# Performance work log

Measured on AMD Instinct MI355X. Metric: run time of the kernel, lower is better.

The kernel has to match this reference:

```python
import jax, jax.numpy as jnp
import numpy as np

B, S, D, H, M, K = 2048, 32, 1024, 1024, 4096, 32


def setup_inputs() -> dict:
    key = jax.random.key(0)
    ks = jax.random.split(key, 10)
    inp = {
        "x": jax.random.normal(ks[0], (B, S, D), dtype=jnp.float32),
        "topk": K,
        "W_enc": jax.random.normal(ks[1], (D, H), dtype=jnp.float32) * (1.0 / np.sqrt(D)),
        "b_enc": jnp.zeros((H,), dtype=jnp.float32),
        "w_curv": jax.random.normal(ks[2], (H, 1), dtype=jnp.float32) * (1.0 / np.sqrt(H)),
        "b_curv": jnp.zeros((1,), dtype=jnp.float32),
        "memory_slots": jax.random.normal(ks[3], (M, H), dtype=jnp.float32),
        "assoc": jax.random.normal(ks[4], (M, M), dtype=jnp.float32) * 0.01,
        "W_dec": jax.random.normal(ks[5], (H, D), dtype=jnp.float32) * (1.0 / np.sqrt(H)),
        "b_dec": jnp.zeros((D,), dtype=jnp.float32),
        "temperature": jnp.asarray(1.0, dtype=jnp.float32),
    }
    return inp


def reference(x, topk, W_enc, b_enc, w_curv, b_curv, memory_slots, assoc, W_dec, b_dec, temperature):
    # encoder + pooled query
    enc = jnp.tanh(x @ W_enc + b_enc)          # [B,S,H]
    query = enc.mean(axis=1)                   # [B,H]

    # content-based addressing (active_slots == M, temperature buffer)
    sim = jnp.einsum('bd,md->bm', query, memory_slots)        # [B,M]
    gate = jax.nn.sigmoid(query @ w_curv + b_curv)            # [B,1]
    sim = sim * (0.5 + gate) / jnp.maximum(temperature, 1e-6)
    vals, idx = jax.lax.top_k(sim, topk)                      # [B,K], sorted desc (matches torch.topk)

    # associative activation: two rounds of softmax -> assoc matmul
    act = jnp.einsum('bd,md->bm', query, memory_slots)        # [B,M]
    for _ in range(2):
        act = jax.nn.softmax(act, axis=-1) @ assoc

    # combine top-k scores with gathered associative activations
    comb = jax.nn.softmax(vals + jnp.take_along_axis(act, idx, axis=1), axis=-1)  # [B,K]
    mem = memory_slots[idx]                                   # [B,K,H] gather
    read = jnp.einsum('bk,bkh->bh', comb, mem)                # [B,H]

    out = jnp.tanh(read @ W_dec + b_dec)                      # [B,D]
    return jnp.broadcast_to(out[:, None, :], (x.shape[0], x.shape[1], out.shape[-1]))
```

## Files before the change

kernel.cpp:

```cpp
#include <hip/hip_runtime.h>

typedef _Float16 f16;
typedef f16 f16x8 __attribute__((ext_vector_type(8)));
typedef float f32x4 __attribute__((ext_vector_type(4)));

#define BD 2048
#define SD 32
#define DD 1024
#define HD 1024
#define MD 4096
#define KD 32
#define PADK 40

__global__ void k_transpose_f16(const float* __restrict__ in, f16* __restrict__ out,
                                int R, int C) {
  __shared__ float tile[32][33];
  int c0 = blockIdx.x * 32, r0 = blockIdx.y * 32;
  int tx = threadIdx.x & 31, ty = threadIdx.x >> 5;
#pragma unroll
  for (int i = 0; i < 4; ++i) {
    int r = ty + i * 8;
    tile[r][tx] = in[(size_t)(r0 + r) * C + c0 + tx];
  }
  __syncthreads();
#pragma unroll
  for (int i = 0; i < 4; ++i) {
    int r = ty + i * 8;
    out[(size_t)(c0 + r) * R + r0 + tx] = (f16)tile[tx][r];
  }
}

__global__ void k_transpose_split(const float* __restrict__ in, f16* __restrict__ outHi,
                                  f16* __restrict__ outLo, int R, int C) {
  __shared__ float tile[32][33];
  int c0 = blockIdx.x * 32, r0 = blockIdx.y * 32;
  int tx = threadIdx.x & 31, ty = threadIdx.x >> 5;
#pragma unroll
  for (int i = 0; i < 4; ++i) {
    int r = ty + i * 8;
    tile[r][tx] = in[(size_t)(r0 + r) * C + c0 + tx];
  }
  __syncthreads();
#pragma unroll
  for (int i = 0; i < 4; ++i) {
    int r = ty + i * 8;
    float v = tile[tx][r];
    f16 h = (f16)v;
    size_t o = (size_t)(c0 + r) * R + r0 + tx;
    outHi[o] = h;
    outLo[o] = (f16)(v - (float)h);
  }
}

__global__ void k_split(const float* __restrict__ in, f16* __restrict__ hi,
                        f16* __restrict__ lo, int n8) {
  int i = blockIdx.x * 256 + threadIdx.x;
  if (i >= n8) return;
  const float4* p = (const float4*)in + (size_t)i * 2;
  float4 a = p[0], b = p[1];
  float v[8] = {a.x, a.y, a.z, a.w, b.x, b.y, b.z, b.w};
  f16x8 h, l;
#pragma unroll
  for (int e = 0; e < 8; ++e) {
    h[e] = (f16)v[e];
    l[e] = (f16)(v[e] - (float)h[e]);
  }
  *((f16x8*)hi + i) = h;
  *((f16x8*)lo + i) = l;
}

template <int SPLIT, int EPI>
__global__ __launch_bounds__(256) void k_gemm_nt(const void* __restrict__ Ap,
                                                 const f16* __restrict__ Bhi,
                                                 const f16* __restrict__ Blo,
                                                 float* __restrict__ C,
                                                 const float* __restrict__ bias,
                                                 int M, int N, int K) {
  __shared__ f16 As[128 * PADK];
  __shared__ f16 Bs[128 * PADK];
  __shared__ f16 Asl[SPLIT ? 128 * PADK : 8];
  __shared__ f16 Bsl[SPLIT ? 128 * PADK : 8];
  const int n0 = blockIdx.x * 128, m0 = blockIdx.y * 128;
  const int t = threadIdx.x;
  const int lane = t & 63, w = t >> 6;
  const int wm = w >> 1, wn = w & 1;
  const int quad = lane >> 4, l16 = lane & 15;
  const int srow = t >> 2, sseg = t & 3;

  f32x4 acc[4][4] = {};

  for (int kc = 0; kc < K; kc += 32) {
#pragma unroll
    for (int rep = 0; rep < 2; ++rep) {
      int row = srow + rep * 64;
      if (SPLIT) {
        const float* g = (const float*)Ap + (size_t)(m0 + row) * K + kc + sseg * 8;
        float4 u0 = *(const float4*)g;
        float4 u1 = *(const float4*)(g + 4);
        float v[8] = {u0.x, u0.y, u0.z, u0.w, u1.x, u1.y, u1.z, u1.w};
        f16x8 h, l;
#pragma unroll
        for (int e = 0; e < 8; ++e) {
          h[e] = (f16)v[e];
          l[e] = (f16)(v[e] - (float)h[e]);
        }
        *(f16x8*)(As + row * PADK + sseg * 8) = h;
        *(f16x8*)(Asl + row * PADK + sseg * 8) = l;
        size_t bo = (size_t)(n0 + row) * K + kc + sseg * 8;
        *(f16x8*)(Bs + row * PADK + sseg * 8) = *(const f16x8*)(Bhi + bo);
        *(f16x8*)(Bsl + row * PADK + sseg * 8) = *(const f16x8*)(Blo + bo);
      } else {
        const f16* g = (const f16*)Ap + (size_t)(m0 + row) * K + kc + sseg * 8;
        *(f16x8*)(As + row * PADK + sseg * 8) = *(const f16x8*)g;
        const f16* gb = Bhi + (size_t)(n0 + row) * K + kc + sseg * 8;
        *(f16x8*)(Bs + row * PADK + sseg * 8) = *(const f16x8*)gb;
      }
    }
    __syncthreads();
    f16x8 ah[4], bh[4];
#pragma unroll
    for (int i = 0; i < 4; ++i) {
      ah[i] = *(const f16x8*)(As + (wm * 64 + i * 16 + l16) * PADK + quad * 8);
      bh[i] = *(const f16x8*)(Bs + (wn * 64 + i * 16 + l16) * PADK + quad * 8);
    }
    if (SPLIT) {
      f16x8 al[4], bl[4];
#pragma unroll
      for (int i = 0; i < 4; ++i) {
        al[i] = *(const f16x8*)(Asl + (wm * 64 + i * 16 + l16) * PADK + quad * 8);
        bl[i] = *(const f16x8*)(Bsl + (wn * 64 + i * 16 + l16) * PADK + quad * 8);
      }
#pragma unroll
      for (int i = 0; i < 4; ++i)
#pragma unroll
        for (int j = 0; j < 4; ++j) {
          acc[i][j] = __builtin_amdgcn_mfma_f32_16x16x32_f16(ah[i], bh[j], acc[i][j], 0, 0, 0);
          acc[i][j] = __builtin_amdgcn_mfma_f32_16x16x32_f16(ah[i], bl[j], acc[i][j], 0, 0, 0);
          acc[i][j] = __builtin_amdgcn_mfma_f32_16x16x32_f16(al[i], bh[j], acc[i][j], 0, 0, 0);
        }
    } else {
#pragma unroll
      for (int i = 0; i < 4; ++i)
#pragma unroll
        for (int j = 0; j < 4; ++j)
          acc[i][j] = __builtin_amdgcn_mfma_f32_16x16x32_f16(ah[i], bh[j], acc[i][j], 0, 0, 0);
    }
    __syncthreads();
  }

  if (EPI == 0) {
#pragma unroll
    for (int i = 0; i < 4; ++i) {
#pragma unroll
      for (int j = 0; j < 4; ++j) {
        int row = m0 + wm * 64 + i * 16 + quad * 4;
        int col = n0 + wn * 64 + j * 16 + l16;
        float* cp = C + (size_t)row * N + col;
#pragma unroll
        for (int r = 0; r < 4; ++r) cp[(size_t)r * N] = acc[i][j][r];
      }
    }
  } else if (EPI == 2) {
#pragma unroll
    for (int i = 0; i < 4; ++i) {
#pragma unroll
      for (int j = 0; j < 4; ++j) {
        int row = m0 + wm * 64 + i * 16 + quad * 4;
        int col = n0 + wn * 64 + j * 16 + l16;
        float bv = bias[col];
        float* cp = C + (size_t)row * N + col;
#pragma unroll
        for (int r = 0; r < 4; ++r) cp[(size_t)r * N] = tanhf(acc[i][j][r] + bv);
      }
    }
  } else {
#pragma unroll
    for (int j = 0; j < 4; ++j) {
      int col = n0 + wn * 64 + j * 16 + l16;
      float bv = bias[col];
      float g0 = 0.f, g1 = 0.f;
#pragma unroll
      for (int i = 0; i < 4; ++i) {
        float s = 0.f;
#pragma unroll
        for (int r = 0; r < 4; ++r) s += tanhf(acc[i][j][r] + bv);
        if (i < 2) g0 += s; else g1 += s;
      }
      g0 += __shfl_xor(g0, 16); g0 += __shfl_xor(g0, 32);
      g1 += __shfl_xor(g1, 16); g1 += __shfl_xor(g1, 32);
      if (quad == 0) {
        int grp = (m0 + wm * 64) >> 5;
        C[(size_t)grp * N + col] = g0 * (1.0f / 32.0f);
        C[(size_t)(grp + 1) * N + col] = g1 * (1.0f / 32.0f);
      }
    }
  }
}

__global__ void k_gate(const float* __restrict__ query, const float* __restrict__ w_curv,
                       const float* __restrict__ b_curv, const float* __restrict__ temp,
                       float* __restrict__ scale) {
  int b = blockIdx.x, t = threadIdx.x;
  float s = 0.f;
  for (int h = t; h < HD; h += 256) s += query[(size_t)b * HD + h] * w_curv[h];
#pragma unroll
  for (int off = 32; off; off >>= 1) s += __shfl_xor(s, off);
  __shared__ float red[4];
  if ((t & 63) == 0) red[t >> 6] = s;
  __syncthreads();
  if (t == 0) {
    float tot = red[0] + red[1] + red[2] + red[3] + b_curv[0];
    float g = 1.f / (1.f + expf(-tot));
    scale[b] = (0.5f + g) / fmaxf(temp[0], 1e-6f);
  }
}

__global__ void k_topk(const float* __restrict__ sim, const float* __restrict__ scale,
                       int* __restrict__ idx, float* __restrict__ vals) {
  int b = blockIdx.x, t = threadIdx.x;
  __shared__ float sv[MD];
  __shared__ float rv[4];
  __shared__ int ri[4];
  for (int i = t; i < MD; i += 256) sv[i] = sim[(size_t)b * MD + i];
  __syncthreads();
  float sc = scale[b];
  for (int k = 0; k < KD; ++k) {
    float bv = -1e30f;
    int bi = 0x7fffffff;
    for (int i = t; i < MD; i += 256) {
      float v = sv[i];
      if (v > bv) { bv = v; bi = i; }
    }
#pragma unroll
    for (int off = 1; off < 64; off <<= 1) {
      float ov = __shfl_xor(bv, off);
      int oi = __shfl_xor(bi, off);
      if (ov > bv || (ov == bv && oi < bi)) { bv = ov; bi = oi; }
    }
    if ((t & 63) == 0) { rv[t >> 6] = bv; ri[t >> 6] = bi; }
    __syncthreads();
    if (t == 0) {
      float fv = rv[0];
      int fi = ri[0];
#pragma unroll
      for (int u = 1; u < 4; ++u)
        if (rv[u] > fv || (rv[u] == fv && ri[u] < fi)) { fv = rv[u]; fi = ri[u]; }
      idx[b * KD + k] = fi;
      vals[b * KD + k] = fv * sc;
      sv[fi] = -1e30f;
    }
    __syncthreads();
  }
}

__global__ void k_softmax(const float* __restrict__ in, f16* __restrict__ out, int C) {
  int b = blockIdx.x, t = threadIdx.x;
  const float* row = in + (size_t)b * C;
  __shared__ float red[4];
  float m = -1e30f;
  for (int i = t; i < C; i += 256) m = fmaxf(m, row[i]);
#pragma unroll
  for (int off = 32; off; off >>= 1) m = fmaxf(m, __shfl_xor(m, off));
  if ((t & 63) == 0) red[t >> 6] = m;
  __syncthreads();
  m = fmaxf(fmaxf(red[0], red[1]), fmaxf(red[2], red[3]));
  __syncthreads();
  float s = 0.f;
  for (int i = t; i < C; i += 256) s += expf(row[i] - m);
#pragma unroll
  for (int off = 32; off; off >>= 1) s += __shfl_xor(s, off);
  if ((t & 63) == 0) red[t >> 6] = s;
  __syncthreads();
  s = red[0] + red[1] + red[2] + red[3];
  float inv = 1.f / s;
  for (int i = t; i < C; i += 256) out[(size_t)b * C + i] = (f16)(expf(row[i] - m) * inv);
}

__global__ void k_combine(const float* __restrict__ vals, const int* __restrict__ idx,
                          const float* __restrict__ act, const float* __restrict__ mem,
                          f16* __restrict__ read_h) {
  int b = blockIdx.x, t = threadIdx.x;
  __shared__ float comb[KD];
  __shared__ int sidx[KD];
  if (t < KD) {
    int id = idx[b * KD + t];
    sidx[t] = id;
    float e = vals[b * KD + t] + act[(size_t)b * MD + id];
    float m = e;
#pragma unroll
    for (int off = 16; off; off >>= 1) m = fmaxf(m, __shfl_xor(m, off));
    float p = expf(e - m);
    float s = p;
#pragma unroll
    for (int off = 16; off; off >>= 1) s += __shfl_xor(s, off);
    comb[t] = p / s;
  }
  __syncthreads();
  for (int h = t; h < HD; h += 256) {
    float a = 0.f;
#pragma unroll
    for (int k = 0; k < KD; ++k) a += comb[k] * mem[(size_t)sidx[k] * HD + h];
    read_h[(size_t)b * HD + h] = (f16)a;
  }
}

__global__ void k_broadcast(const float4* __restrict__ src, float4* __restrict__ dst) {
  size_t v = (size_t)blockIdx.x * 256 + threadIdx.x;
  size_t d4 = v & 255;
  size_t b = v >> 13;
  dst[v] = src[b * 256 + d4];
}

extern "C" void kernel_launch(void* const* d_in, const int* in_sizes, int n_in,
                              void* d_out, int out_size, void* d_ws, size_t ws_size,
                              hipStream_t stream) {
  const float* x      = (const float*)d_in[0];
  const float* W_enc  = (const float*)d_in[2];
  const float* b_enc  = (const float*)d_in[3];
  const float* w_curv = (const float*)d_in[4];
  const float* b_curv = (const float*)d_in[5];
  const float* mem    = (const float*)d_in[6];
  const float* assoc  = (const float*)d_in[7];
  const float* W_dec  = (const float*)d_in[8];
  const float* b_dec  = (const float*)d_in[9];
  const float* temp   = (const float*)d_in[10];
  float* out = (float*)d_out;

  char* ws = (char*)d_ws;
  size_t off = 0;
  auto alloc = [&](size_t bytes) {
    void* p = ws + off;
    off += (bytes + 255) & ~(size_t)255;
    return p;
  };
  f16* Wt_hi   = (f16*)alloc((size_t)HD * DD * 2);
  f16* Wt_lo   = (f16*)alloc((size_t)HD * DD * 2);
  f16* ms_hi   = (f16*)alloc((size_t)MD * HD * 2);
  f16* ms_lo   = (f16*)alloc((size_t)MD * HD * 2);
  f16* assocT  = (f16*)alloc((size_t)MD * MD * 2);
  f16* WdT     = (f16*)alloc((size_t)DD * HD * 2);
  float* query = (float*)alloc((size_t)BD * HD * 4);
  float* scale = (float*)alloc((size_t)BD * 4);
  float* sim   = (float*)alloc((size_t)BD * MD * 4);
  int* idx     = (int*)alloc((size_t)BD * KD * 4);
  float* vals  = (float*)alloc((size_t)BD * KD * 4);
  f16* p_h     = (f16*)alloc((size_t)BD * MD * 2);
  f16* read_h  = (f16*)alloc((size_t)BD * HD * 2);
  float* out_b = (float*)alloc((size_t)BD * DD * 4);
  (void)ws_size; (void)in_sizes; (void)n_in; (void)out_size;

  dim3 b256(256);
  k_transpose_split<<<dim3(HD / 32, DD / 32), b256, 0, stream>>>(W_enc, Wt_hi, Wt_lo, DD, HD);
  k_split<<<dim3((MD * HD / 8 + 255) / 256), b256, 0, stream>>>(mem, ms_hi, ms_lo, MD * HD / 8);
  k_transpose_f16<<<dim3(MD / 32, MD / 32), b256, 0, stream>>>(assoc, assocT, MD, MD);
  k_transpose_f16<<<dim3(DD / 32, HD / 32), b256, 0, stream>>>(W_dec, WdT, HD, DD);
  k_gemm_nt<1, 1><<<dim3(HD / 128, BD * SD / 128), b256, 0, stream>>>(
      x, Wt_hi, Wt_lo, query, b_enc, BD * SD, HD, DD);
  k_gate<<<dim3(BD), b256, 0, stream>>>(query, w_curv, b_curv, temp, scale);
  k_gemm_nt<1, 0><<<dim3(MD / 128, BD / 128), b256, 0, stream>>>(
      query, ms_hi, ms_lo, sim, nullptr, BD, MD, HD);
  k_topk<<<dim3(BD), b256, 0, stream>>>(sim, scale, idx, vals);
  k_softmax<<<dim3(BD), b256, 0, stream>>>(sim, p_h, MD);
  k_gemm_nt<0, 0><<<dim3(MD / 128, BD / 128), b256, 0, stream>>>(
      p_h, assocT, nullptr, sim, nullptr, BD, MD, MD);
  k_softmax<<<dim3(BD), b256, 0, stream>>>(sim, p_h, MD);
  k_gemm_nt<0, 0><<<dim3(MD / 128, BD / 128), b256, 0, stream>>>(
      p_h, assocT, nullptr, sim, nullptr, BD, MD, MD);
  k_combine<<<dim3(BD), b256, 0, stream>>>(vals, idx, sim, mem, read_h);
  k_gemm_nt<0, 2><<<dim3(DD / 128, BD / 128), b256, 0, stream>>>(
      read_h, WdT, nullptr, out_b, b_dec, BD, DD, HD);
  k_broadcast<<<dim3(BD * SD * DD / 1024), b256, 0, stream>>>(
      (const float4*)out_b, (float4*)out);
}
```

Before: 1.461 ms.

## Prepack B operands in MFMA fragment layout and fuse decoder broadcast

Weights and memory slots are prepacked into the per-lane MFMA fragment order, so the GEMM loads B fragments straight from global memory into registers and no longer stages them through LDS. The A tile in LDS uses an XOR swizzle instead of padding to avoid bank conflicts. The final decoder GEMM writes the tanh output broadcast across S directly, which removes the intermediate buffer and the separate broadcast kernel. The trade-off is that B fragments are now read from global memory by every wave without LDS sharing, which adds cache traffic. The fused epilogue also writes its output with strided, less coalesced stores.

```diff
diff --git a/kernel.cpp b/kernel.cpp
--- a/kernel.cpp
+++ b/kernel.cpp
@@ -10,89 +10,87 @@
 #define HD 1024
 #define MD 4096
 #define KD 32
-#define PADK 40
-
-__global__ void k_transpose_f16(const float* __restrict__ in, f16* __restrict__ out,
-                                int R, int C) {
-  __shared__ float tile[32][33];
-  int c0 = blockIdx.x * 32, r0 = blockIdx.y * 32;
-  int tx = threadIdx.x & 31, ty = threadIdx.x >> 5;
-#pragma unroll
-  for (int i = 0; i < 4; ++i) {
-    int r = ty + i * 8;
-    tile[r][tx] = in[(size_t)(r0 + r) * C + c0 + tx];
-  }
-  __syncthreads();
-#pragma unroll
-  for (int i = 0; i < 4; ++i) {
-    int r = ty + i * 8;
-    out[(size_t)(c0 + r) * R + r0 + tx] = (f16)tile[tx][r];
-  }
-}
-
-__global__ void k_transpose_split(const float* __restrict__ in, f16* __restrict__ outHi,
-                                  f16* __restrict__ outLo, int R, int C) {
-  __shared__ float tile[32][33];
-  int c0 = blockIdx.x * 32, r0 = blockIdx.y * 32;
-  int tx = threadIdx.x & 31, ty = threadIdx.x >> 5;
-#pragma unroll
-  for (int i = 0; i < 4; ++i) {
-    int r = ty + i * 8;
-    tile[r][tx] = in[(size_t)(r0 + r) * C + c0 + tx];
-  }
-  __syncthreads();
-#pragma unroll
-  for (int i = 0; i < 4; ++i) {
-    int r = ty + i * 8;
-    float v = tile[tx][r];
-    f16 h = (f16)v;
-    size_t o = (size_t)(c0 + r) * R + r0 + tx;
-    outHi[o] = h;
-    outLo[o] = (f16)(v - (float)h);
-  }
-}
-
-__global__ void k_split(const float* __restrict__ in, f16* __restrict__ hi,
-                        f16* __restrict__ lo, int n8) {
-  int i = blockIdx.x * 256 + threadIdx.x;
-  if (i >= n8) return;
-  const float4* p = (const float4*)in + (size_t)i * 2;
-  float4 a = p[0], b = p[1];
-  float v[8] = {a.x, a.y, a.z, a.w, b.x, b.y, b.z, b.w};
+
+__global__ void k_pack_rows(const float* __restrict__ in, f16* __restrict__ hi,
+                            f16* __restrict__ lo, int N, int K) {
+  int t = blockIdx.x * 256 + threadIdx.x;
+  int total = (N >> 4) * (K >> 5) * 64;
+  if (t >= total) return;
+  int l16 = t & 15, quad = (t >> 4) & 3;
+  int x = t >> 6;
+  int kch = K >> 5;
+  int kc = x % kch, nt = x / kch;
+  const float* src = in + (size_t)(nt * 16 + l16) * K + kc * 32 + quad * 8;
+  float4 u0 = *(const float4*)src;
+  float4 u1 = *(const float4*)(src + 4);
+  float v[8] = {u0.x, u0.y, u0.z, u0.w, u1.x, u1.y, u1.z, u1.w};
   f16x8 h, l;
 #pragma unroll
   for (int e = 0; e < 8; ++e) {
     h[e] = (f16)v[e];
     l[e] = (f16)(v[e] - (float)h[e]);
   }
-  *((f16x8*)hi + i) = h;
-  *((f16x8*)lo + i) = l;
+  ((f16x8*)hi)[t] = h;
+  if (lo) ((f16x8*)lo)[t] = l;
+}
+
+__global__ void k_pack_T(const float* __restrict__ in, f16* __restrict__ hi,
+                         f16* __restrict__ lo, int N, int K) {
+  int t = blockIdx.x * 256 + threadIdx.x;
+  int total = (N >> 4) * (K >> 5) * 64;
+  if (t >= total) return;
+  int l16 = t & 15, quad = (t >> 4) & 3;
+  int x = t >> 6;
+  int kch = K >> 5;
+  int kc = x % kch, nt = x / kch;
+  int col = nt * 16 + l16;
+  int krow = kc * 32 + quad * 8;
+  f16x8 h, l;
+#pragma unroll
+  for (int e = 0; e < 8; ++e) {
+    float v = in[(size_t)(krow + e) * N + col];
+    f16 hh = (f16)v;
+    h[e] = hh;
+    l[e] = (f16)(v - (float)hh);
+  }
+  ((f16x8*)hi)[t] = h;
+  if (lo) ((f16x8*)lo)[t] = l;
 }
 
 template <int SPLIT, int EPI>
-__global__ __launch_bounds__(256) void k_gemm_nt(const void* __restrict__ Ap,
-                                                 const f16* __restrict__ Bhi,
-                                                 const f16* __restrict__ Blo,
-                                                 float* __restrict__ C,
-                                                 const float* __restrict__ bias,
-                                                 int M, int N, int K) {
-  __shared__ f16 As[128 * PADK];
-  __shared__ f16 Bs[128 * PADK];
-  __shared__ f16 Asl[SPLIT ? 128 * PADK : 8];
-  __shared__ f16 Bsl[SPLIT ? 128 * PADK : 8];
+__global__ __launch_bounds__(256) void k_gemm(const void* __restrict__ Ap,
+                                              const f16* __restrict__ Bhi,
+                                              const f16* __restrict__ Blo,
+                                              float* __restrict__ C,
+                                              const float* __restrict__ bias,
+                                              int M, int N, int K) {
+  __shared__ f16 As[128 * 32];
+  __shared__ f16 Asl[SPLIT ? 128 * 32 : 8];
   const int n0 = blockIdx.x * 128, m0 = blockIdx.y * 128;
   const int t = threadIdx.x;
   const int lane = t & 63, w = t >> 6;
   const int wm = w >> 1, wn = w & 1;
   const int quad = lane >> 4, l16 = lane & 15;
   const int srow = t >> 2, sseg = t & 3;
+  const int swf = (srow >> 1) & 3;
+  const int rwf = (l16 >> 1) & 3;
+  const int kch = K >> 5;
 
   f32x4 acc[4][4] = {};
 
-  for (int kc = 0; kc < K; kc += 32) {
+  for (int kc32 = 0; kc32 < kch; ++kc32) {
+    const int kc = kc32 << 5;
+    f16x8 bh[4], bl[4];
+#pragma unroll
+    for (int j = 0; j < 4; ++j) {
+      size_t fi = (((size_t)((n0 >> 4) + wn * 4 + j) * kch + kc32) << 6) + (quad << 4) + l16;
+      bh[j] = ((const f16x8*)Bhi)[fi];
+      if (SPLIT) bl[j] = ((const f16x8*)Blo)[fi];
+    }
 #pragma unroll
     for (int rep = 0; rep < 2; ++rep) {
       int row = srow + rep * 64;
+      int slot = row * 32 + ((sseg ^ swf) << 3);
       if (SPLIT) {
         const float* g = (const float*)Ap + (size_t)(m0 + row) * K + kc + sseg * 8;
         float4 u0 = *(const float4*)g;
@@ -104,32 +102,22 @@
           h[e] = (f16)v[e];
           l[e] = (f16)(v[e] - (float)h[e]);
         }
-        *(f16x8*)(As + row * PADK + sseg * 8) = h;
-        *(f16x8*)(Asl + row * PADK + sseg * 8) = l;
-        size_t bo = (size_t)(n0 + row) * K + kc + sseg * 8;
-        *(f16x8*)(Bs + row * PADK + sseg * 8) = *(const f16x8*)(Bhi + bo);
-        *(f16x8*)(Bsl + row * PADK + sseg * 8) = *(const f16x8*)(Blo + bo);
+        *(f16x8*)(As + slot) = h;
+        *(f16x8*)(Asl + slot) = l;
       } else {
         const f16* g = (const f16*)Ap + (size_t)(m0 + row) * K + kc + sseg * 8;
-        *(f16x8*)(As + row * PADK + sseg * 8) = *(const f16x8*)g;
-        const f16* gb = Bhi + (size_t)(n0 + row) * K + kc + sseg * 8;
-        *(f16x8*)(Bs + row * PADK + sseg * 8) = *(const f16x8*)gb;
+        *(f16x8*)(As + slot) = *(const f16x8*)g;
       }
     }
     __syncthreads();
-    f16x8 ah[4], bh[4];
+    f16x8 ah[4], al[4];
 #pragma unroll
     for (int i = 0; i < 4; ++i) {
-      ah[i] = *(const f16x8*)(As + (wm * 64 + i * 16 + l16) * PADK + quad * 8);
-      bh[i] = *(const f16x8*)(Bs + (wn * 64 + i * 16 + l16) * PADK + quad * 8);
+      int off = (wm * 64 + i * 16 + l16) * 32 + ((quad ^ rwf) << 3);
+      ah[i] = *(const f16x8*)(As + off);
+      if (SPLIT) al[i] = *(const f16x8*)(Asl + off);
     }
     if (SPLIT) {
-      f16x8 al[4], bl[4];
-#pragma unroll
-      for (int i = 0; i < 4; ++i) {
-        al[i] = *(const f16x8*)(Asl + (wm * 64 + i * 16 + l16) * PADK + quad * 8);
-        bl[i] = *(const f16x8*)(Bsl + (wn * 64 + i * 16 + l16) * PADK + quad * 8);
-      }
 #pragma unroll
       for (int i = 0; i < 4; ++i)
 #pragma unroll
@@ -171,6 +159,24 @@
         float* cp = C + (size_t)row * N + col;
 #pragma unroll
         for (int r = 0; r < 4; ++r) cp[(size_t)r * N] = tanhf(acc[i][j][r] + bv);
+      }
+    }
+  } else if (EPI == 3) {
+#pragma unroll
+    for (int i = 0; i < 4; ++i) {
+#pragma unroll
+      for (int j = 0; j < 4; ++j) {
+        int row = m0 + wm * 64 + i * 16 + quad * 4;
+        int col = n0 + wn * 64 + j * 16 + l16;
+        float bv = bias[col];
+        float vv[4];
+#pragma unroll
+        for (int r = 0; r < 4; ++r) vv[r] = tanhf(acc[i][j][r] + bv);
+        for (int s = 0; s < SD; ++s) {
+          float* cp = C + ((size_t)row * SD + s) * N + col;
+#pragma unroll
+          for (int r = 0; r < 4; ++r) cp[(size_t)r * SD * N] = vv[r];
+        }
       }
     }
   } else {
@@ -302,13 +308,6 @@
     for (int k = 0; k < KD; ++k) a += comb[k] * mem[(size_t)sidx[k] * HD + h];
     read_h[(size_t)b * HD + h] = (f16)a;
   }
-}
-
-__global__ void k_broadcast(const float4* __restrict__ src, float4* __restrict__ dst) {
-  size_t v = (size_t)blockIdx.x * 256 + threadIdx.x;
-  size_t d4 = v & 255;
-  size_t b = v >> 13;
-  dst[v] = src[b * 256 + d4];
 }
 
 extern "C" void kernel_launch(void* const* d_in, const int* in_sizes, int n_in,
@@ -337,8 +336,8 @@
   f16* Wt_lo   = (f16*)alloc((size_t)HD * DD * 2);
   f16* ms_hi   = (f16*)alloc((size_t)MD * HD * 2);
   f16* ms_lo   = (f16*)alloc((size_t)MD * HD * 2);
-  f16* assocT  = (f16*)alloc((size_t)MD * MD * 2);
-  f16* WdT     = (f16*)alloc((size_t)DD * HD * 2);
+  f16* as_pk   = (f16*)alloc((size_t)MD * MD * 2);
+  f16* wd_pk   = (f16*)alloc((size_t)HD * DD * 2);
   float* query = (float*)alloc((size_t)BD * HD * 4);
   float* scale = (float*)alloc((size_t)BD * 4);
   float* sim   = (float*)alloc((size_t)BD * MD * 4);
@@ -346,29 +345,26 @@
   float* vals  = (float*)alloc((size_t)BD * KD * 4);
   f16* p_h     = (f16*)alloc((size_t)BD * MD * 2);
   f16* read_h  = (f16*)alloc((size_t)BD * HD * 2);
-  float* out_b = (float*)alloc((size_t)BD * DD * 4);
   (void)ws_size; (void)in_sizes; (void)n_in; (void)out_size;
 
   dim3 b256(256);
-  k_transpose_split<<<dim3(HD / 32, DD / 32), b256, 0, stream>>>(W_enc, Wt_hi, Wt_lo, DD, HD);
-  k_split<<<dim3((MD * HD / 8 + 255) / 256), b256, 0, stream>>>(mem, ms_hi, ms_lo, MD * HD / 8);
-  k_transpose_f16<<<dim3(MD / 32, MD / 32), b256, 0, stream>>>(assoc, assocT, MD, MD);
-  k_transpose_f16<<<dim3(DD / 32, HD / 32), b256, 0, stream>>>(W_dec, WdT, HD, DD);
-  k_gemm_nt<1, 1><<<dim3(HD / 128, BD * SD / 128), b256, 0, stream>>>(
+  k_pack_T<<<dim3((HD / 16) * (DD / 32) * 64 / 256), b256, 0, stream>>>(W_enc, Wt_hi, Wt_lo, HD, DD);
+  k_pack_rows<<<dim3((MD / 16) * (HD / 32) * 64 / 256), b256, 0, stream>>>(mem, ms_hi, ms_lo, MD, HD);
+  k_pack_T<<<dim3((MD / 16) * (MD / 32) * 64 / 256), b256, 0, stream>>>(assoc, as_pk, nullptr, MD, MD);
+  k_pack_T<<<dim3((DD / 16) * (HD / 32) * 64 / 256), b256, 0, stream>>>(W_dec, wd_pk, nullptr, DD, HD);
+  k_gemm<1, 1><<<dim3(HD / 128, BD * SD / 128), b256, 0, stream>>>(
       x, Wt_hi, Wt_lo, query, b_enc, BD * SD, HD, DD);
   k_gate<<<dim3(BD), b256, 0, stream>>>(query, w_curv, b_curv, temp, scale);
-  k_gemm_nt<1, 0><<<dim3(MD / 128, BD / 128), b256, 0, stream>>>(
+  k_gemm<1, 0><<<dim3(MD / 128, BD / 128), b256, 0, stream>>>(
       query, ms_hi, ms_lo, sim, nullptr, BD, MD, HD);
   k_topk<<<dim3(BD), b256, 0, stream>>>(sim, scale, idx, vals);
   k_softmax<<<dim3(BD), b256, 0, stream>>>(sim, p_h, MD);
-  k_gemm_nt<0, 0><<<dim3(MD / 128, BD / 128), b256, 0, stream>>>(
-      p_h, assocT, nullptr, sim, nullptr, BD, MD, MD);
+  k_gemm<0, 0><<<dim3(MD / 128, BD / 128), b256, 0, stream>>>(
+      p_h, as_pk, nullptr, sim, nullptr, BD, MD, MD);
   k_softmax<<<dim3(BD), b256, 0, stream>>>(sim, p_h, MD);
-  k_gemm_nt<0, 0><<<dim3(MD / 128, BD / 128), b256, 0, stream>>>(
-      p_h, assocT, nullptr, sim, nullptr, BD, MD, MD);
+  k_gemm<0, 0><<<dim3(MD / 128, BD / 128), b256, 0, stream>>>(
+      p_h, as_pk, nullptr, sim, nullptr, BD, MD, MD);
   k_combine<<<dim3(BD), b256, 0, stream>>>(vals, idx, sim, mem, read_h);
-  k_gemm_nt<0, 2><<<dim3(DD / 128, BD / 128), b256, 0, stream>>>(
-      read_h, WdT, nullptr, out_b, b_dec, BD, DD, HD);
-  k_broadcast<<<dim3(BD * SD * DD / 1024), b256, 0, stream>>>(
-      (const float4*)out_b, (float4*)out);
-}
+  k_gemm<0, 3><<<dim3(DD / 128, BD / 128), b256, 0, stream>>>(
+      read_h, wd_pk, nullptr, out, b_dec, BD, DD, HD);
+}
```

Result: faster. 1.407 ms (-3.6%).
